# Performance work log

Hardware: AMD Instinct MI355X
Metric: run time of the kernel (lower is better)

The kernel has to match this reference:

```python
import jax, jax.numpy as jnp
import numpy as np

NUM_HEADS = 12


def setup_inputs() -> dict:
    key = jax.random.key(0)
    k1, k2, k3 = jax.random.split(key, 3)
    B, S, D = 8, 1024, 768
    x = jax.random.normal(k1, (B, S, D), dtype=jnp.float32)
    # Linear weights, torch convention [out_features, in_features], small init
    w_qkv = jax.random.normal(k2, (3 * D, D), dtype=jnp.float32) * 0.02
    b_qkv = jnp.zeros((3 * D,), dtype=jnp.float32)
    w_proj = jax.random.normal(k3, (D, D), dtype=jnp.float32) * 0.02
    b_proj = jnp.zeros((D,), dtype=jnp.float32)
    return {"x": x, "w_qkv": w_qkv, "b_qkv": b_qkv, "w_proj": w_proj, "b_proj": b_proj}


def reference(x, w_qkv, b_qkv, w_proj, b_proj):
    B, S, D = x.shape
    H = NUM_HEADS
    hd = D // H
    qkv = x @ w_qkv.T + b_qkv                      # [B, S, 3D]
    qkv = qkv.reshape(B, S, 3, H, hd).transpose(2, 0, 3, 1, 4)  # [3, B, H, S, hd]
    q, k, v = qkv[0], qkv[1], qkv[2]
    # NOTE: source computes self.scale but never applies it -> unscaled QK^T
    weights = jnp.einsum('bhqd,bhkd->bhqk', q, k)  # [B, H, S, S]
    attn = jax.nn.softmax(weights, axis=-1)        # dropout = 0 (eval)
    out = jnp.einsum('bhqk,bhkd->bhqd', attn, v)   # [B, H, S, hd]
    out = out.transpose(0, 2, 1, 3).reshape(B, S, D)
    return out @ w_proj.T + b_proj
```

## Files before the change

### kernel.cpp

```cpp
#include <hip/hip_runtime.h>


typedef short bf16x8 __attribute__((ext_vector_type(8)));
typedef float f32x4  __attribute__((ext_vector_type(4)));

#define MFMA16(a, b, c) __builtin_amdgcn_mfma_f32_16x16x32_bf16((a), (b), (c), 0, 0, 0)

__device__ __forceinline__ unsigned short f2bf(float f) {
    union { float f; unsigned int u; } v; v.f = f;
    unsigned int u = v.u;
    return (unsigned short)((u + 0x7fffu + ((u >> 16) & 1u)) >> 16);
}

__device__ __forceinline__ unsigned int cvt2(float x, float y) {
#if __has_builtin(__builtin_amdgcn_cvt_pk_bf16_f32)
    auto v = __builtin_amdgcn_cvt_pk_bf16_f32(x, y);
    unsigned int b; __builtin_memcpy(&b, &v, 4); return b;
#else
    return (unsigned int)f2bf(x) | ((unsigned int)f2bf(y) << 16);
#endif
}

__device__ __forceinline__ void gl2lds16(const unsigned short* g, unsigned short* l) {
    __builtin_amdgcn_global_load_lds(
        (const unsigned int __attribute__((address_space(1)))*)g,
        (unsigned int __attribute__((address_space(3)))*)l,
        16, 0, 0);
}

__global__ void cvt3_kernel(const float* __restrict__ x,
                            const float* __restrict__ wq,
                            const float* __restrict__ wp,
                            unsigned short* __restrict__ xb,
                            unsigned short* __restrict__ wqb,
                            unsigned short* __restrict__ wpb) {
    int i = blockIdx.x * 256 + threadIdx.x;
    const float* s; unsigned short* d; int off;
    if (i < 1572864)      { s = x;  d = xb;  off = i; }
    else if (i < 2015232) { s = wq; d = wqb; off = i - 1572864; }
    else                  { s = wp; d = wpb; off = i - 2015232; }
    float4 v = ((const float4*)s)[off];
    ushort4 o;
    o.x = f2bf(v.x); o.y = f2bf(v.y); o.z = f2bf(v.z); o.w = f2bf(v.w);
    ((ushort4*)d)[off] = o;
}

__global__ __launch_bounds__(256) void gemm_qkv(
    const unsigned short* __restrict__ A,
    const unsigned short* __restrict__ Bm,
    const float* __restrict__ bias,
    unsigned short* __restrict__ Qo,
    unsigned short* __restrict__ Ko,
    unsigned short* __restrict__ Vto) {
    const int K = 768;
    __shared__ __align__(16) unsigned short smem[16384];
    unsigned short* Asv[2] = { smem, smem + 4096 };
    unsigned short* Bsv[2] = { smem + 8192, smem + 12288 };
    const int tid = threadIdx.x;
    const int wave = tid >> 6, lane = tid & 63;
    const int quad = lane >> 4, l16 = lane & 15;
    const int wm = (wave >> 1) * 64, wn = (wave & 1) * 64;
    const int tileM = blockIdx.x * 128, tileN = blockIdx.y * 128;

    f32x4 zero4 = {0.f, 0.f, 0.f, 0.f};
    f32x4 acc[4][4];
#pragma unroll
    for (int i = 0; i < 4; ++i)
#pragma unroll
        for (int j = 0; j < 4; ++j) acc[i][j] = zero4;

    const unsigned short* Ab = A + (size_t)tileM * K;
    const unsigned short* Bb = Bm + (size_t)tileN * K;

    for (int k0 = 0; k0 < K; k0 += 64) {
#pragma unroll
        for (int i = 0; i < 2; ++i) {
            int s = tid + (i << 8);
            int r = s >> 2, c = s & 3;
            const unsigned short* ga = Ab + (size_t)r * K + k0 + c * 8;
            const unsigned short* gb = Bb + (size_t)r * K + k0 + c * 8;
            int dst = ((wave << 6) + (i << 8)) * 8;
            gl2lds16(ga,      Asv[0] + dst);
            gl2lds16(ga + 32, Asv[1] + dst);
            gl2lds16(gb,      Bsv[0] + dst);
            gl2lds16(gb + 32, Bsv[1] + dst);
        }
        __syncthreads();
#pragma unroll
        for (int ks = 0; ks < 2; ++ks) {
            bf16x8 af[4], bfr[4];
#pragma unroll
            for (int t = 0; t < 4; ++t) {
                af[t]  = *(const bf16x8*)(Asv[ks] + (wm + t * 16 + l16) * 32 + quad * 8);
                bfr[t] = *(const bf16x8*)(Bsv[ks] + (wn + t * 16 + l16) * 32 + quad * 8);
            }
#pragma unroll
            for (int tm = 0; tm < 4; ++tm)
#pragma unroll
                for (int tn = 0; tn < 4; ++tn)
                    acc[tm][tn] = MFMA16(af[tm], bfr[tn], acc[tm][tn]);
        }
        __syncthreads();
    }

    const int t = blockIdx.y / 6;
    if (t < 2) {
        const float scale = (t == 0) ? 1.44269504f : 1.0f;
        unsigned short* dst = (t == 0) ? Qo : Ko;
        const int nb = tileN - t * 768 + wn;
#pragma unroll
        for (int tm = 0; tm < 4; ++tm) {
#pragma unroll
            for (int tn = 0; tn < 4; ++tn) {
                int nl = nb + tn * 16 + l16;
                float bv = bias[tileN + wn + tn * 16 + l16];
#pragma unroll
                for (int r = 0; r < 4; ++r) {
                    int m = tileM + wm + tm * 16 + quad * 4 + r;
                    dst[(size_t)m * 768 + nl] = f2bf((acc[tm][tn][r] + bv) * scale);
                }
            }
        }
    } else {
        const int b = tileM >> 10, srow = tileM & 1023;
#pragma unroll
        for (int h2 = 0; h2 < 2; ++h2) {
            __syncthreads();
            if ((wn >> 6) == h2) {
#pragma unroll
                for (int tn = 0; tn < 4; ++tn) {
                    int dl = tn * 16 + l16;
                    float bv = bias[tileN + wn + dl];
#pragma unroll
                    for (int tm = 0; tm < 4; ++tm) {
                        int mb = wm + tm * 16 + quad * 4;
                        uint2 pk;
                        pk.x = cvt2(acc[tm][tn][0] + bv, acc[tm][tn][1] + bv);
                        pk.y = cvt2(acc[tm][tn][2] + bv, acc[tm][tn][3] + bv);
                        *(uint2*)(smem + dl * 136 + mb) = pk;
                    }
                }
            }
            __syncthreads();
#pragma unroll
            for (int pass = 0; pass < 4; ++pass) {
                int dl = pass * 16 + (tid >> 4), soff = (tid & 15) * 8;
                bf16x8 row = *(const bf16x8*)(smem + dl * 136 + soff);
                int rem = tileN + h2 * 64 + dl - 1536;
                int h = rem >> 6, d = rem & 63;
                *(bf16x8*)(Vto + (((size_t)b * 12 + h) * 64 + d) * 1024 + srow + soff) = row;
            }
        }
    }
}

__global__ __launch_bounds__(256) void attn_kernel(
    const unsigned short* __restrict__ Q,
    const unsigned short* __restrict__ Kg,
    const unsigned short* __restrict__ Vt,
    unsigned short* __restrict__ O) {
    __shared__ __align__(16) unsigned short smem[16384];
    unsigned short* Ps  = smem;
    unsigned short* Qsv[2] = { smem, smem + 4096 };
    unsigned short* Ksv[2] = { smem + 8192,  smem + 10240 };
    unsigned short* Vsv[2] = { smem + 12288, smem + 14336 };

    const int tid = threadIdx.x;
    const int wave = tid >> 6, lane = tid & 63;
    const int quad = lane >> 4, l16 = lane & 15;
    const int s4 = l16 & 3;
    const int qt = blockIdx.x;
    const int bh = blockIdx.y;
    const int b = bh / 12, h = bh - b * 12;

    const unsigned short* Qb = Q  + ((size_t)b * 1024 + qt * 128) * 768 + h * 64;
    const unsigned short* Kb = Kg + (size_t)b * 1024 * 768 + h * 64;
    const unsigned short* Vb = Vt + (size_t)bh * 64 * 1024;

#pragma unroll
    for (int i = 0; i < 2; ++i) {
        int s = tid + (i << 8);
        int r = s >> 2, c = s & 3;
        const unsigned short* gq = Qb + (size_t)r * 768 + c * 8;
        int dst = ((wave << 6) + (i << 8)) * 8;
        gl2lds16(gq,      Qsv[0] + dst);
        gl2lds16(gq + 32, Qsv[1] + dst);
    }
    __syncthreads();
    bf16x8 qf[2][2];
#pragma unroll
    for (int ks = 0; ks < 2; ++ks)
#pragma unroll
        for (int tq = 0; tq < 2; ++tq)
            qf[ks][tq] = *(const bf16x8*)(Qsv[ks] + (wave * 32 + tq * 16 + l16) * 32 + quad * 8);
    __syncthreads();

    f32x4 zero4 = {0.f, 0.f, 0.f, 0.f};
    f32x4 oacc[2][4];
    float rsum[2] = {0.f, 0.f};
#pragma unroll
    for (int tm = 0; tm < 2; ++tm)
#pragma unroll
        for (int tv = 0; tv < 4; ++tv) oacc[tm][tv] = zero4;

    for (int kv0 = 0; kv0 < 1024; kv0 += 64) {
        {
            int r = tid >> 2, c = tid & 3;
            const unsigned short* gk = Kb + (size_t)(kv0 + r) * 768 + c * 8;
            const unsigned short* gv = Vb + (size_t)r * 1024 + kv0 + c * 8;
            int dst = (wave << 6) * 8;
            gl2lds16(gk,      Ksv[0] + dst);
            gl2lds16(gk + 32, Ksv[1] + dst);
            gl2lds16(gv,      Vsv[0] + dst);
            gl2lds16(gv + 32, Vsv[1] + dst);
        }
        __syncthreads();

        f32x4 st[4][2];
#pragma unroll
        for (int tk = 0; tk < 4; ++tk)
#pragma unroll
            for (int tq = 0; tq < 2; ++tq) st[tk][tq] = zero4;
#pragma unroll
        for (int ks = 0; ks < 2; ++ks) {
            bf16x8 kf[4];
#pragma unroll
            for (int tk = 0; tk < 4; ++tk)
                kf[tk] = *(const bf16x8*)(Ksv[ks] + (tk * 16 + l16) * 32 + quad * 8);
#pragma unroll
            for (int tk = 0; tk < 4; ++tk)
#pragma unroll
                for (int tq = 0; tq < 2; ++tq)
                    st[tk][tq] = MFMA16(kf[tk], qf[ks][tq], st[tk][tq]);
        }

#pragma unroll
        for (int tq = 0; tq < 2; ++tq) {
            unsigned short* prp = Ps + (wave * 32 + tq * 16 + l16) * 64 + quad * 4;
#pragma unroll
            for (int tk = 0; tk < 4; ++tk) {
                float e0 = __builtin_amdgcn_exp2f(st[tk][tq][0]);
                float e1 = __builtin_amdgcn_exp2f(st[tk][tq][1]);
                float e2 = __builtin_amdgcn_exp2f(st[tk][tq][2]);
                float e3 = __builtin_amdgcn_exp2f(st[tk][tq][3]);
                rsum[tq] += (e0 + e1) + (e2 + e3);
                uint2 pk;
                pk.x = cvt2(e0, e1);
                pk.y = cvt2(e2, e3);
                *(uint2*)(prp + ((tk ^ s4) << 4)) = pk;
            }
        }

#pragma unroll
        for (int ks2 = 0; ks2 < 2; ++ks2) {
            bf16x8 ap[2], bv[4];
            int colswz = ((ks2 << 5) + (quad << 3)) ^ (s4 << 4);
#pragma unroll
            for (int tm = 0; tm < 2; ++tm)
                ap[tm] = *(const bf16x8*)(Ps + (wave * 32 + tm * 16 + l16) * 64 + colswz);
#pragma unroll
            for (int tv = 0; tv < 4; ++tv)
                bv[tv] = *(const bf16x8*)(Vsv[ks2] + (tv * 16 + l16) * 32 + quad * 8);
#pragma unroll
            for (int tm = 0; tm < 2; ++tm)
#pragma unroll
                for (int tv = 0; tv < 4; ++tv)
                    oacc[tm][tv] = MFMA16(ap[tm], bv[tv], oacc[tm][tv]);
        }
        __syncthreads();
    }

#pragma unroll
    for (int tq = 0; tq < 2; ++tq) {
        rsum[tq] += __shfl_xor(rsum[tq], 16, 64);
        rsum[tq] += __shfl_xor(rsum[tq], 32, 64);
    }
    float* sums = (float*)smem;
    if (quad == 0) {
        sums[wave * 32 + l16]      = rsum[0];
        sums[wave * 32 + 16 + l16] = rsum[1];
    }
    __syncthreads();

#pragma unroll
    for (int tm = 0; tm < 2; ++tm) {
        f32x4 inv;
#pragma unroll
        for (int r = 0; r < 4; ++r)
            inv[r] = 1.0f / sums[wave * 32 + tm * 16 + quad * 4 + r];
#pragma unroll
        for (int tv = 0; tv < 4; ++tv)
#pragma unroll
            for (int r = 0; r < 4; ++r) {
                int srow = qt * 128 + wave * 32 + tm * 16 + quad * 4 + r;
                int col = h * 64 + tv * 16 + l16;
                O[((size_t)b * 1024 + srow) * 768 + col] = f2bf(oacc[tm][tv][r] * inv[r]);
            }
    }
}

__global__ __launch_bounds__(256) void gemm_proj(
    const unsigned short* __restrict__ A,
    const unsigned short* __restrict__ Bm,
    const float* __restrict__ bias,
    float* __restrict__ out) {
    const int K = 768;
    __shared__ __align__(16) unsigned short smem[16384];
    unsigned short* Asv[2] = { smem, smem + 4096 };
    unsigned short* Bsv[2] = { smem + 8192, smem + 12288 };
    const int tid = threadIdx.x;
    const int wave = tid >> 6, lane = tid & 63;
    const int quad = lane >> 4, l16 = lane & 15;
    const int wm = (wave >> 1) * 64, wn = (wave & 1) * 64;
    const int tileM = blockIdx.x * 128, tileN = blockIdx.y * 128;

    f32x4 zero4 = {0.f, 0.f, 0.f, 0.f};
    f32x4 acc[4][4];
#pragma unroll
    for (int i = 0; i < 4; ++i)
#pragma unroll
        for (int j = 0; j < 4; ++j) acc[i][j] = zero4;

    const unsigned short* Ab = A + (size_t)tileM * K;
    const unsigned short* Bb = Bm + (size_t)tileN * K;

    for (int k0 = 0; k0 < K; k0 += 64) {
#pragma unroll
        for (int i = 0; i < 2; ++i) {
            int s = tid + (i << 8);
            int r = s >> 2, c = s & 3;
            const unsigned short* ga = Ab + (size_t)r * K + k0 + c * 8;
            const unsigned short* gb = Bb + (size_t)r * K + k0 + c * 8;
            int dst = ((wave << 6) + (i << 8)) * 8;
            gl2lds16(ga,      Asv[0] + dst);
            gl2lds16(ga + 32, Asv[1] + dst);
            gl2lds16(gb,      Bsv[0] + dst);
            gl2lds16(gb + 32, Bsv[1] + dst);
        }
        __syncthreads();
#pragma unroll
        for (int ks = 0; ks < 2; ++ks) {
            bf16x8 af[4], bfr[4];
#pragma unroll
            for (int t = 0; t < 4; ++t) {
                af[t]  = *(const bf16x8*)(Asv[ks] + (wm + t * 16 + l16) * 32 + quad * 8);
                bfr[t] = *(const bf16x8*)(Bsv[ks] + (wn + t * 16 + l16) * 32 + quad * 8);
            }
#pragma unroll
            for (int tm = 0; tm < 4; ++tm)
#pragma unroll
                for (int tn = 0; tn < 4; ++tn)
                    acc[tm][tn] = MFMA16(af[tm], bfr[tn], acc[tm][tn]);
        }
        __syncthreads();
    }

#pragma unroll
    for (int tm = 0; tm < 4; ++tm) {
#pragma unroll
        for (int tn = 0; tn < 4; ++tn) {
            int n = tileN + wn + tn * 16 + l16;
            float bv = bias[n];
#pragma unroll
            for (int r = 0; r < 4; ++r) {
                int m = tileM + wm + tm * 16 + quad * 4 + r;
                out[(size_t)m * 768 + n] = acc[tm][tn][r] + bv;
            }
        }
    }
}

extern "C" void kernel_launch(void* const* d_in, const int* in_sizes, int n_in,
                              void* d_out, int out_size, void* d_ws, size_t ws_size,
                              hipStream_t stream) {
    (void)in_sizes; (void)n_in; (void)out_size; (void)ws_size;
    const float* x      = (const float*)d_in[0];
    const float* w_qkv  = (const float*)d_in[1];
    const float* b_qkv  = (const float*)d_in[2];
    const float* w_proj = (const float*)d_in[3];
    const float* b_proj = (const float*)d_in[4];
    float* out = (float*)d_out;

    char* ws = (char*)d_ws;
    unsigned short* xb     = (unsigned short*)(ws + 0);
    unsigned short* wqkvb  = (unsigned short*)(ws + 12582912);
    unsigned short* wprojb = (unsigned short*)(ws + 16121856);
    unsigned short* Qw     = (unsigned short*)(ws + 17301504);
    unsigned short* Kw     = (unsigned short*)(ws + 29884416);
    unsigned short* Vtw    = (unsigned short*)(ws + 42467328);

    cvt3_kernel<<<8448, 256, 0, stream>>>(x, w_qkv, w_proj, xb, wqkvb, wprojb);
    gemm_qkv<<<dim3(64, 18), 256, 0, stream>>>(xb, wqkvb, b_qkv, Qw, Kw, Vtw);
    attn_kernel<<<dim3(8, 96), 256, 0, stream>>>(Qw, Kw, Vtw, xb);
    gemm_proj<<<dim3(64, 6), 256, 0, stream>>>(xb, wprojb, b_proj, out);
}
```

Baseline: 224.1 us.

## Double-buffer global-to-LDS loads in GEMMs and attention KV loop

Both GEMM kernels now use two LDS buffers of 32-wide K slices. Each iteration issues the async global-to-LDS copy for the next slice before running the MFMAs on the current one, so only one barrier per step is needed. The attention kernel likewise prefetches the next K/V tile into a second buffer while computing on the current tile, which grows its LDS to 48KB. The aim is to hide global-load latency behind matrix math. The risks are lower occupancy in attention, twice as many barriers in the GEMMs, and reliance on barriers to cover the outstanding async loads.

```diff
diff --git a/kernel.cpp b/kernel.cpp
--- a/kernel.cpp
+++ b/kernel.cpp
@@ -54,8 +54,6 @@
     unsigned short* __restrict__ Vto) {
     const int K = 768;
     __shared__ __align__(16) unsigned short smem[16384];
-    unsigned short* Asv[2] = { smem, smem + 4096 };
-    unsigned short* Bsv[2] = { smem + 8192, smem + 12288 };
     const int tid = threadIdx.x;
     const int wave = tid >> 6, lane = tid & 63;
     const int quad = lane >> 4, l16 = lane & 15;
@@ -72,35 +70,36 @@
     const unsigned short* Ab = A + (size_t)tileM * K;
     const unsigned short* Bb = Bm + (size_t)tileN * K;
 
-    for (int k0 = 0; k0 < K; k0 += 64) {
+    auto stage = [&](int k0, int buf) {
+        unsigned short* Ad = smem + buf * 4096;
+        unsigned short* Bd = smem + 8192 + buf * 4096;
 #pragma unroll
         for (int i = 0; i < 2; ++i) {
             int s = tid + (i << 8);
             int r = s >> 2, c = s & 3;
-            const unsigned short* ga = Ab + (size_t)r * K + k0 + c * 8;
-            const unsigned short* gb = Bb + (size_t)r * K + k0 + c * 8;
             int dst = ((wave << 6) + (i << 8)) * 8;
-            gl2lds16(ga,      Asv[0] + dst);
-            gl2lds16(ga + 32, Asv[1] + dst);
-            gl2lds16(gb,      Bsv[0] + dst);
-            gl2lds16(gb + 32, Bsv[1] + dst);
-        }
+            gl2lds16(Ab + (size_t)r * K + k0 + c * 8, Ad + dst);
+            gl2lds16(Bb + (size_t)r * K + k0 + c * 8, Bd + dst);
+        }
+    };
+
+    stage(0, 0);
+    for (int it = 0; it < 24; ++it) {
         __syncthreads();
-#pragma unroll
-        for (int ks = 0; ks < 2; ++ks) {
-            bf16x8 af[4], bfr[4];
-#pragma unroll
-            for (int t = 0; t < 4; ++t) {
-                af[t]  = *(const bf16x8*)(Asv[ks] + (wm + t * 16 + l16) * 32 + quad * 8);
-                bfr[t] = *(const bf16x8*)(Bsv[ks] + (wn + t * 16 + l16) * 32 + quad * 8);
-            }
-#pragma unroll
-            for (int tm = 0; tm < 4; ++tm)
-#pragma unroll
-                for (int tn = 0; tn < 4; ++tn)
-                    acc[tm][tn] = MFMA16(af[tm], bfr[tn], acc[tm][tn]);
-        }
-        __syncthreads();
+        if (it + 1 < 24) stage((it + 1) << 5, (it + 1) & 1);
+        const unsigned short* Ar = smem + (it & 1) * 4096;
+        const unsigned short* Br = smem + 8192 + (it & 1) * 4096;
+        bf16x8 af[4], bfr[4];
+#pragma unroll
+        for (int t = 0; t < 4; ++t) {
+            af[t]  = *(const bf16x8*)(Ar + (wm + t * 16 + l16) * 32 + quad * 8);
+            bfr[t] = *(const bf16x8*)(Br + (wn + t * 16 + l16) * 32 + quad * 8);
+        }
+#pragma unroll
+        for (int tm = 0; tm < 4; ++tm)
+#pragma unroll
+            for (int tn = 0; tn < 4; ++tn)
+                acc[tm][tn] = MFMA16(af[tm], bfr[tn], acc[tm][tn]);
     }
 
     const int t = blockIdx.y / 6;
@@ -159,11 +158,8 @@
     const unsigned short* __restrict__ Kg,
     const unsigned short* __restrict__ Vt,
     unsigned short* __restrict__ O) {
-    __shared__ __align__(16) unsigned short smem[16384];
-    unsigned short* Ps  = smem;
-    unsigned short* Qsv[2] = { smem, smem + 4096 };
-    unsigned short* Ksv[2] = { smem + 8192,  smem + 10240 };
-    unsigned short* Vsv[2] = { smem + 12288, smem + 14336 };
+    __shared__ __align__(16) unsigned short smem[24576];
+    unsigned short* Ps = smem;
 
     const int tid = threadIdx.x;
     const int wave = tid >> 6, lane = tid & 63;
@@ -177,22 +173,37 @@
     const unsigned short* Kb = Kg + (size_t)b * 1024 * 768 + h * 64;
     const unsigned short* Vb = Vt + (size_t)bh * 64 * 1024;
 
+    auto stageKV = [&](int kv0, int buf) {
+        int r = tid >> 2, c = tid & 3;
+        const unsigned short* gk = Kb + (size_t)(kv0 + r) * 768 + c * 8;
+        const unsigned short* gv = Vb + (size_t)r * 1024 + kv0 + c * 8;
+        unsigned short* Kd = smem + 8192 + buf * 4096;
+        unsigned short* Vd = smem + 16384 + buf * 4096;
+        int dst = (wave << 6) * 8;
+        gl2lds16(gk,      Kd + dst);
+        gl2lds16(gk + 32, Kd + 2048 + dst);
+        gl2lds16(gv,      Vd + dst);
+        gl2lds16(gv + 32, Vd + 2048 + dst);
+    };
+
 #pragma unroll
     for (int i = 0; i < 2; ++i) {
         int s = tid + (i << 8);
         int r = s >> 2, c = s & 3;
         const unsigned short* gq = Qb + (size_t)r * 768 + c * 8;
         int dst = ((wave << 6) + (i << 8)) * 8;
-        gl2lds16(gq,      Qsv[0] + dst);
-        gl2lds16(gq + 32, Qsv[1] + dst);
-    }
+        gl2lds16(gq,      smem + dst);
+        gl2lds16(gq + 32, smem + 4096 + dst);
+    }
+    stageKV(0, 0);
     __syncthreads();
     bf16x8 qf[2][2];
 #pragma unroll
     for (int ks = 0; ks < 2; ++ks)
 #pragma unroll
         for (int tq = 0; tq < 2; ++tq)
-            qf[ks][tq] = *(const bf16x8*)(Qsv[ks] + (wave * 32 + tq * 16 + l16) * 32 + quad * 8);
+            qf[ks][tq] = *(const bf16x8*)(smem + ks * 4096 +
+                                          (wave * 32 + tq * 16 + l16) * 32 + quad * 8);
     __syncthreads();
 
     f32x4 zero4 = {0.f, 0.f, 0.f, 0.f};
@@ -203,18 +214,10 @@
 #pragma unroll
         for (int tv = 0; tv < 4; ++tv) oacc[tm][tv] = zero4;
 
-    for (int kv0 = 0; kv0 < 1024; kv0 += 64) {
-        {
-            int r = tid >> 2, c = tid & 3;
-            const unsigned short* gk = Kb + (size_t)(kv0 + r) * 768 + c * 8;
-            const unsigned short* gv = Vb + (size_t)r * 1024 + kv0 + c * 8;
-            int dst = (wave << 6) * 8;
-            gl2lds16(gk,      Ksv[0] + dst);
-            gl2lds16(gk + 32, Ksv[1] + dst);
-            gl2lds16(gv,      Vsv[0] + dst);
-            gl2lds16(gv + 32, Vsv[1] + dst);
-        }
-        __syncthreads();
+    for (int it = 0; it < 16; ++it) {
+        if (it + 1 < 16) stageKV((it + 1) << 6, (it + 1) & 1);
+        const unsigned short* Kr = smem + 8192 + (it & 1) * 4096;
+        const unsigned short* Vr = smem + 16384 + (it & 1) * 4096;
 
         f32x4 st[4][2];
 #pragma unroll
@@ -226,7 +229,7 @@
             bf16x8 kf[4];
 #pragma unroll
             for (int tk = 0; tk < 4; ++tk)
-                kf[tk] = *(const bf16x8*)(Ksv[ks] + (tk * 16 + l16) * 32 + quad * 8);
+                kf[tk] = *(const bf16x8*)(Kr + ks * 2048 + (tk * 16 + l16) * 32 + quad * 8);
 #pragma unroll
             for (int tk = 0; tk < 4; ++tk)
 #pragma unroll
@@ -260,7 +263,7 @@
                 ap[tm] = *(const bf16x8*)(Ps + (wave * 32 + tm * 16 + l16) * 64 + colswz);
 #pragma unroll
             for (int tv = 0; tv < 4; ++tv)
-                bv[tv] = *(const bf16x8*)(Vsv[ks2] + (tv * 16 + l16) * 32 + quad * 8);
+                bv[tv] = *(const bf16x8*)(Vr + ks2 * 2048 + (tv * 16 + l16) * 32 + quad * 8);
 #pragma unroll
             for (int tm = 0; tm < 2; ++tm)
 #pragma unroll
@@ -306,8 +309,6 @@
     float* __restrict__ out) {
     const int K = 768;
     __shared__ __align__(16) unsigned short smem[16384];
-    unsigned short* Asv[2] = { smem, smem + 4096 };
-    unsigned short* Bsv[2] = { smem + 8192, smem + 12288 };
     const int tid = threadIdx.x;
     const int wave = tid >> 6, lane = tid & 63;
     const int quad = lane >> 4, l16 = lane & 15;
@@ -324,35 +325,36 @@
     const unsigned short* Ab = A + (size_t)tileM * K;
     const unsigned short* Bb = Bm + (size_t)tileN * K;
 
-    for (int k0 = 0; k0 < K; k0 += 64) {
+    auto stage = [&](int k0, int buf) {
+        unsigned short* Ad = smem + buf * 4096;
+        unsigned short* Bd = smem + 8192 + buf * 4096;
 #pragma unroll
         for (int i = 0; i < 2; ++i) {
             int s = tid + (i << 8);
             int r = s >> 2, c = s & 3;
-            const unsigned short* ga = Ab + (size_t)r * K + k0 + c * 8;
-            const unsigned short* gb = Bb + (size_t)r * K + k0 + c * 8;
             int dst = ((wave << 6) + (i << 8)) * 8;
-            gl2lds16(ga,      Asv[0] + dst);
-            gl2lds16(ga + 32, Asv[1] + dst);
-            gl2lds16(gb,      Bsv[0] + dst);
-            gl2lds16(gb + 32, Bsv[1] + dst);
-        }
+            gl2lds16(Ab + (size_t)r * K + k0 + c * 8, Ad + dst);
+            gl2lds16(Bb + (size_t)r * K + k0 + c * 8, Bd + dst);
+        }
+    };
+
+    stage(0, 0);
+    for (int it = 0; it < 24; ++it) {
         __syncthreads();
-#pragma unroll
-        for (int ks = 0; ks < 2; ++ks) {
-            bf16x8 af[4], bfr[4];
-#pragma unroll
-            for (int t = 0; t < 4; ++t) {
-                af[t]  = *(const bf16x8*)(Asv[ks] + (wm + t * 16 + l16) * 32 + quad * 8);
-                bfr[t] = *(const bf16x8*)(Bsv[ks] + (wn + t * 16 + l16) * 32 + quad * 8);
-            }
-#pragma unroll
-            for (int tm = 0; tm < 4; ++tm)
-#pragma unroll
-                for (int tn = 0; tn < 4; ++tn)
-                    acc[tm][tn] = MFMA16(af[tm], bfr[tn], acc[tm][tn]);
-        }
-        __syncthreads();
+        if (it + 1 < 24) stage((it + 1) << 5, (it + 1) & 1);
+        const unsigned short* Ar = smem + (it & 1) * 4096;
+        const unsigned short* Br = smem + 8192 + (it & 1) * 4096;
+        bf16x8 af[4], bfr[4];
+#pragma unroll
+        for (int t = 0; t < 4; ++t) {
+            af[t]  = *(const bf16x8*)(Ar + (wm + t * 16 + l16) * 32 + quad * 8);
+            bfr[t] = *(const bf16x8*)(Br + (wn + t * 16 + l16) * 32 + quad * 8);
+        }
+#pragma unroll
+        for (int tm = 0; tm < 4; ++tm)
+#pragma unroll
+            for (int tn = 0; tn < 4; ++tn)
+                acc[tm][tn] = MFMA16(af[tm], bfr[tn], acc[tm][tn]);
     }
 
 #pragma unroll
```

After: 200.0 us. -10.8%, faster.
